# Performance work log

Measured on AMD Instinct MI355X. Metric: run time of the kernel, lower is better.

Reference implementation:

```python
import jax, jax.numpy as jnp
import numpy as np

B, S, N, F_RAW = 32, 48, 1000, 21
H = 64           # hidden_dim
A_DIM = 10       # aspect_dim
FEAT = 4 * A_DIM # projected feature_dim = 40

OFF_IDX = np.array([2, 5, 8, 9, 12])
DEF_IDX = np.array([10, 14, 15])
ERR_IDX = np.array([13, 17])
INF_IDX = np.array([19, 20])


def _glorot(k, shape):
    lim = (6.0 / (shape[0] + shape[1])) ** 0.5
    return jax.random.uniform(k, shape, minval=-lim, maxval=lim, dtype=jnp.float32)


def setup_inputs() -> dict:
    key = jax.random.key(0)
    ks = jax.random.split(key, 12)
    return {
        'inputs': jax.random.normal(ks[0], (B, S, N, F_RAW), dtype=jnp.float32),
        'adj': jax.random.uniform(ks[1], (N, N), dtype=jnp.float32),
        # aspect projection linears (weight stored as [in, out])
        'Wo': _glorot(ks[2], (5, A_DIM)), 'bo': jnp.zeros((A_DIM,), jnp.float32),
        'Wd': _glorot(ks[3], (3, A_DIM)), 'bd': jnp.zeros((A_DIM,), jnp.float32),
        'We': _glorot(ks[4], (2, A_DIM)), 'be': jnp.zeros((A_DIM,), jnp.float32),
        'Wi': _glorot(ks[5], (2, A_DIM)), 'bi': jnp.zeros((A_DIM,), jnp.float32),
        # graph-conv GRU weights: gates (bias init 1.0) and candidate (bias 0.0)
        'W1': _glorot(ks[6], (H + FEAT, 2 * H)), 'b1': jnp.ones((2 * H,), jnp.float32),
        'W2': _glorot(ks[7], (H + FEAT, H)), 'b2': jnp.zeros((H,), jnp.float32),
    }


def _laplacian_with_self_loop(adj):
    A = adj + jnp.eye(adj.shape[0], dtype=adj.dtype)
    d_inv_sqrt = A.sum(axis=1) ** -0.5
    return d_inv_sqrt[:, None] * A * d_inv_sqrt[None, :]


def reference(inputs, adj, Wo, bo, Wd, bd, We, be, Wi, bi, W1, b1, W2, b2):
    b, s, n, _ = inputs.shape
    L = _laplacian_with_self_loop(adj)  # [N, N]

    # vectorized per-node aspect projections -> [B, S, N, 40]
    x = jnp.concatenate([
        inputs[..., OFF_IDX] @ Wo + bo,
        inputs[..., DEF_IDX] @ Wd + bd,
        inputs[..., ERR_IDX] @ We + be,
        inputs[..., INF_IDX] @ Wi + bi,
    ], axis=-1)

    def gconv(x_t, h_flat, W, bias, out_dim):
        # x_t: [B, N, FEAT]; h_flat: [B, N*H]
        cat = jnp.concatenate([x_t, h_flat.reshape(b, n, H)], axis=-1)  # [B,N,H+FEAT]
        ag = jnp.einsum('mn,bnf->bmf', L, cat)                          # [B,N,H+FEAT]
        out = ag @ W + bias                                             # [B,N,out_dim]
        return out.reshape(b, n * out_dim)

    def step(h_flat, x_t):
        # NOTE: chunk over the flattened (B, N*2H) axis, as in the torch code
        ru = jax.nn.sigmoid(gconv(x_t, h_flat, W1, b1, 2 * H))  # [B, N*2H]
        r, u = jnp.split(ru, 2, axis=1)                          # each [B, N*H]
        c = jnp.tanh(gconv(x_t, r * h_flat, W2, b2, H))          # [B, N*H]
        h_new = u * h_flat + (1.0 - u) * c
        return h_new, None

    h0 = jnp.zeros((b, n * H), dtype=inputs.dtype)
    h_last, _ = jax.lax.scan(step, h0, jnp.swapaxes(x, 0, 1))  # scan over seq
    return h_last.reshape(b, n, H)
```

## Files before the change

### kernel.cpp

```cpp
#include <hip/hip_runtime.h>
#include <math.h>

#define NN    1000
#define KP    1024
#define BATCH 32
#define SEQ   48
#define HID   64
#define LCOLS 32256

typedef unsigned short u16;
typedef __attribute__((ext_vector_type(8))) short  short8v;
typedef __attribute__((ext_vector_type(8))) unsigned short ushort8v;
typedef __attribute__((ext_vector_type(4))) float  float4v;

__device__ __forceinline__ u16 f2bf(float x) {
    union { float f; unsigned u; } v; v.f = x;
    unsigned r = v.u + 0x7FFF + ((v.u >> 16) & 1);
    return (u16)(r >> 16);
}
__device__ __forceinline__ float bf2f(u16 h) {
    union { unsigned u; float f; } v; v.u = ((unsigned)h) << 16;
    return v.f;
}

__global__ void k_rowsum(const float* __restrict__ adj, float* __restrict__ dinv) {
    int m = blockIdx.x;
    float s = 0.f;
    for (int n = threadIdx.x; n < NN; n += blockDim.x)
        s += adj[(size_t)m*NN + n];
    __shared__ float red[256];
    red[threadIdx.x] = s; __syncthreads();
    for (int st = 128; st > 0; st >>= 1) {
        if (threadIdx.x < st) red[threadIdx.x] += red[threadIdx.x + st];
        __syncthreads();
    }
    if (threadIdx.x == 0) dinv[m] = rsqrtf(red[0] + 1.0f);
}

__global__ void k_buildL(const float* __restrict__ adj, const float* __restrict__ dinv,
                         u16* __restrict__ Lhi) {
    int idx = blockIdx.x * 256 + threadIdx.x;
    if (idx >= KP*KP) return;
    int m = idx >> 10, k = idx & (KP-1);
    float v = 0.f;
    if (m < NN && k < NN)
        v = dinv[m] * (adj[(size_t)m*NN + k] + (m == k ? 1.f : 0.f)) * dinv[k];
    Lhi[idx] = f2bf(v);
}

__global__ void k_buildLf(const float* __restrict__ adj, const float* __restrict__ dinv,
                          u16* __restrict__ Lf) {
    size_t idx = (size_t)blockIdx.x * 256 + threadIdx.x;
    if (idx >= (size_t)KP*KP) return;
    int e    = idx & 7;
    int lane = (idx >> 3) & 63;
    int kb   = (idx >> 9) & 31;
    int mg   = idx >> 14;
    int m = mg*16 + (lane & 15);
    int k = kb*32 + (lane >> 4)*8 + e;
    float v = 0.f;
    if (m < NN && k < NN)
        v = dinv[m] * (adj[(size_t)m*NN + k] + (m == k ? 1.f : 0.f)) * dinv[k];
    Lf[idx] = f2bf(v);
}

__global__ void k_srow(const float* __restrict__ adj, const float* __restrict__ dinv,
                       float* __restrict__ srl) {
    int m = blockIdx.x;
    __shared__ float red[256];
    float s = 0.f;
    if (m < NN)
        for (int n = threadIdx.x; n < NN; n += blockDim.x)
            s += adj[(size_t)m*NN + n] * dinv[n];
    red[threadIdx.x] = s; __syncthreads();
    for (int st = 128; st > 0; st >>= 1) {
        if (threadIdx.x < st) red[threadIdx.x] += red[threadIdx.x + st];
        __syncthreads();
    }
    if (threadIdx.x == 0) srl[m] = (m < NN) ? dinv[m] * (red[0] + dinv[m]) : 0.f;
}

__global__ void k_wconv(const float* __restrict__ W1, const float* __restrict__ W2,
                        u16* __restrict__ W1h, u16* __restrict__ W2h) {
    int idx = blockIdx.x * 256 + threadIdx.x;
    if (idx < 128*128) {
        int k = idx >> 7, f = idx & 127;
        W1h[idx] = f2bf((f < 104) ? W1[f*128 + k] : 0.f);
    } else if (idx < 128*128 + 64*128) {
        int i2 = idx - 128*128;
        int c = i2 >> 7, f = i2 & 127;
        W2h[i2] = f2bf((f < 104) ? W2[f*64 + c] : 0.f);
    }
}

__global__ void k_packW(const float* __restrict__ Wo, const float* __restrict__ bo,
                        const float* __restrict__ Wd, const float* __restrict__ bd,
                        const float* __restrict__ We, const float* __restrict__ be,
                        const float* __restrict__ Wi, const float* __restrict__ bi,
                        float* __restrict__ Wp, float* __restrict__ bp) {
    for (int o = threadIdx.x; o < 21*40; o += 256) {
        int f = o / 40, a = o - f*40;
        int g = a / 10, aa = a - 10*g;
        float v = 0.f;
        if (g == 0) {
            if (f == 2) v = Wo[0*10+aa]; else if (f == 5) v = Wo[1*10+aa];
            else if (f == 8) v = Wo[2*10+aa]; else if (f == 9) v = Wo[3*10+aa];
            else if (f == 12) v = Wo[4*10+aa];
        } else if (g == 1) {
            if (f == 10) v = Wd[aa]; else if (f == 14) v = Wd[10+aa];
            else if (f == 15) v = Wd[20+aa];
        } else if (g == 2) {
            if (f == 13) v = We[aa]; else if (f == 17) v = We[10+aa];
        } else {
            if (f == 19) v = Wi[aa]; else if (f == 20) v = Wi[10+aa];
        }
        Wp[o] = v;
    }
    if (threadIdx.x < 40) {
        int a = threadIdx.x, g = a / 10, aa = a - 10*g;
        bp[a] = (g == 0) ? bo[aa] : (g == 1) ? bd[aa] : (g == 2) ? be[aa] : bi[aa];
    }
}

__global__ __launch_bounds__(256)
void k_transpose(const float* __restrict__ inputs, u16* __restrict__ inT) {
    int bt = blockIdx.x;
    int b = bt / SEQ, t = bt - b*SEQ;
    int nt = blockIdx.y;
    __shared__ float sm[128][22];
    const float* base = inputs + ((size_t)bt * NN + nt*128) * 21;
    for (int i = threadIdx.x; i < 128*21; i += 256) {
        int nn = i / 21, f = i - nn*21;
        int n = nt*128 + nn;
        sm[nn][f] = (n < NN) ? base[(size_t)nn*21 + f] : 0.f;
    }
    __syncthreads();
    for (int o = threadIdx.x; o < 21*128; o += 256) {
        int f = o >> 7, nn = o & 127;
        inT[(size_t)((t*32 + b)*21 + f)*KP + nt*128 + nn] = f2bf(sm[nn][f]);
    }
}

__global__ __launch_bounds__(512)
void k_gemm(const u16* __restrict__ A, const u16* __restrict__ B,
            u16* __restrict__ Cout, int ncols) {
    __shared__ char sA[128*64];
    __shared__ char sB[64*64];
    const int n0 = blockIdx.x * 64;
    const int m0 = blockIdx.y * 128;
    const int tid = threadIdx.x;
    const int w = tid >> 6, lane = tid & 63;
    const int l15 = lane & 15, l4 = lane >> 4;
    const int wm = w >> 1, wn = w & 1;

    float4v acc[2][2];
    #pragma unroll
    for (int i = 0; i < 2; ++i)
        #pragma unroll
        for (int j = 0; j < 2; ++j) acc[i][j] = (float4v){0.f,0.f,0.f,0.f};

    int aoff[2], boff[2];
    #pragma unroll
    for (int mf = 0; mf < 2; ++mf) {
        int r = wm*32 + mf*16 + l15;
        aoff[mf] = (r*64 + l4*16) ^ ((r & 7) << 4);
    }
    #pragma unroll
    for (int nf = 0; nf < 2; ++nf) {
        int r = wn*32 + nf*16 + l15;
        boff[nf] = (r*64 + l4*16) ^ ((r & 7) << 4);
    }
    const int rA = tid >> 2, qA = tid & 3;
    const int dA = (rA*64 + qA*16) ^ ((rA & 7) << 4);
    const size_t gA = (size_t)(m0 + rA)*KP + qA*8;
    const int rB = (tid & 255) >> 2, qB = tid & 3;
    const int dB = (rB*64 + qB*16) ^ ((rB & 7) << 4);
    const size_t gB = (size_t)(n0 + rB)*KP + qB*8;

    for (int kt = 0; kt < 32; ++kt) {
        const int k0 = kt*32;
        __syncthreads();
        *(uint4*)(sA + dA) = *(const uint4*)(A + gA + k0);
        if (tid < 256) *(uint4*)(sB + dB) = *(const uint4*)(B + gB + k0);
        __syncthreads();
        short8v a0 = *(const short8v*)(sA + aoff[0]);
        short8v a1 = *(const short8v*)(sA + aoff[1]);
        short8v b0 = *(const short8v*)(sB + boff[0]);
        short8v b1 = *(const short8v*)(sB + boff[1]);
        acc[0][0] = __builtin_amdgcn_mfma_f32_16x16x32_bf16(a0, b0, acc[0][0], 0, 0, 0);
        acc[0][1] = __builtin_amdgcn_mfma_f32_16x16x32_bf16(a0, b1, acc[0][1], 0, 0, 0);
        acc[1][0] = __builtin_amdgcn_mfma_f32_16x16x32_bf16(a1, b0, acc[1][0], 0, 0, 0);
        acc[1][1] = __builtin_amdgcn_mfma_f32_16x16x32_bf16(a1, b1, acc[1][1], 0, 0, 0);
    }
    #pragma unroll
    for (int mf = 0; mf < 2; ++mf)
        #pragma unroll
        for (int nf = 0; nf < 2; ++nf)
            #pragma unroll
            for (int i = 0; i < 4; ++i) {
                int m = m0 + wm*32 + mf*16 + l4*4 + i;
                int j = n0 + wn*32 + nf*16 + l15;
                Cout[(size_t)m*ncols + j] = f2bf(acc[mf][nf][i]);
            }
}

__device__ __forceinline__ size_t frag_off(int grp, int kb, int lane) {
    return (((size_t)grp*32 + kb)*64 + lane)*8;
}

__global__ __launch_bounds__(256)
void k_g1(const u16* __restrict__ Lf, const u16* __restrict__ hTf,
          const u16* __restrict__ agx, const u16* __restrict__ W1h,
          const float* __restrict__ b1, const float* __restrict__ h_lin,
          u16* __restrict__ rhf, float* __restrict__ u_lin) {
    const int b = blockIdx.x, mt = blockIdx.y;
    const int m0 = mt*64;
    const int tid = threadIdx.x;
    const int w = tid >> 6, lane = tid & 63, l15 = lane & 15, l4 = lane >> 4;
    const int wm = w >> 1, wn = w & 1;

    __shared__ char smem[49408];
    char* sF = smem;
    float* ru_s = (float*)(smem + 16384);

    float4v acc[2][2];
    #pragma unroll
    for (int i = 0; i < 2; ++i)
        #pragma unroll
        for (int j = 0; j < 2; ++j) acc[i][j] = (float4v){0.f,0.f,0.f,0.f};

    const u16* A0 = Lf  + frag_off(mt*4 + wm*2 + 0, 0, lane);
    const u16* A1 = Lf  + frag_off(mt*4 + wm*2 + 1, 0, lane);
    const u16* B0 = hTf + frag_off(b*4  + wn*2 + 0, 0, lane);
    const u16* B1 = hTf + frag_off(b*4  + wn*2 + 1, 0, lane);
    #pragma unroll 8
    for (int kb = 0; kb < 32; ++kb) {
        short8v a0 = *(const short8v*)(A0 + kb*512);
        short8v a1 = *(const short8v*)(A1 + kb*512);
        short8v b0 = *(const short8v*)(B0 + kb*512);
        short8v b1 = *(const short8v*)(B1 + kb*512);
        acc[0][0] = __builtin_amdgcn_mfma_f32_16x16x32_bf16(a0, b0, acc[0][0], 0, 0, 0);
        acc[0][1] = __builtin_amdgcn_mfma_f32_16x16x32_bf16(a0, b1, acc[0][1], 0, 0, 0);
        acc[1][0] = __builtin_amdgcn_mfma_f32_16x16x32_bf16(a1, b0, acc[1][0], 0, 0, 0);
        acc[1][1] = __builtin_amdgcn_mfma_f32_16x16x32_bf16(a1, b1, acc[1][1], 0, 0, 0);
    }

    if (tid < 192) {
        int r = tid / 3, q = tid - 3*(tid/3);
        *(uint4*)(sF + ((r*256 + (13 + q)*16) ^ ((r & 7) << 4))) = (uint4){0,0,0,0};
    }
    for (int i = tid; i < 320; i += 256) {
        int r = i / 5, q = i - 5*(i/5);
        *(uint4*)(sF + ((r*256 + q*16) ^ ((r & 7) << 4))) =
            *(const uint4*)(agx + (size_t)(m0 + r)*1280 + b*40 + q*8);
    }
    #pragma unroll
    for (int mf = 0; mf < 2; ++mf)
        #pragma unroll
        for (int nf = 0; nf < 2; ++nf)
            #pragma unroll
            for (int i = 0; i < 4; ++i) {
                int row = wm*32 + mf*16 + l4*4 + i;
                int f = 40 + wn*32 + nf*16 + l15;
                *(u16*)(sF + ((row*256 + f*2) ^ ((row & 7) << 4))) = f2bf(acc[mf][nf][i]);
            }
    __syncthreads();

    const int gm = (w >> 1)*32, gn = (w & 1)*64;
    float4v acc2[2][4];
    #pragma unroll
    for (int i = 0; i < 2; ++i)
        #pragma unroll
        for (int j = 0; j < 4; ++j) acc2[i][j] = (float4v){0.f,0.f,0.f,0.f};
    for (int kt2 = 0; kt2 < 4; ++kt2) {
        #pragma unroll
        for (int mf = 0; mf < 2; ++mf) {
            int ar2 = gm + mf*16 + l15;
            short8v a = *(const short8v*)(sF + ((ar2*256 + kt2*64 + l4*16) ^ ((ar2 & 7) << 4)));
            #pragma unroll
            for (int nf = 0; nf < 4; ++nf) {
                short8v bb = *(const short8v*)(W1h + (gn + nf*16 + l15)*128 + kt2*32 + l4*8);
                acc2[mf][nf] = __builtin_amdgcn_mfma_f32_16x16x32_bf16(a, bb, acc2[mf][nf], 0, 0, 0);
            }
        }
    }
    #pragma unroll
    for (int mf = 0; mf < 2; ++mf)
        #pragma unroll
        for (int nf = 0; nf < 4; ++nf) {
            int col = gn + nf*16 + l15;
            float bias = b1[col];
            #pragma unroll
            for (int i = 0; i < 4; ++i) {
                int row = gm + mf*16 + l4*4 + i;
                ru_s[row*129 + col] = 1.f / (1.f + __expf(-(acc2[mf][nf][i] + bias)));
            }
        }
    __syncthreads();

    const int c = tid & 63, ng = tid >> 6;
    #pragma unroll
    for (int it = 0; it < 4; ++it) {
        int nc = (it*4 + ng)*8;
        int n = 2*m0 + nc;
        if ((n >> 1) + 3 < 500) {
            ushort8v ov;
            #pragma unroll
            for (int d = 0; d < 8; ++d) {
                int nn = n + d;
                float r = ru_s[((nc + d) >> 1)*129 + (nn & 1)*64 + c];
                float h = h_lin[((size_t)b*NN + nn)*64 + c];
                ov[d] = f2bf(r*h);
            }
            *(ushort8v*)(rhf + frag_off(b*4 + (c >> 4), n >> 5, (c & 15) + 16*((n >> 3) & 3))) = ov;
        }
    }
    for (int lc = 0; lc < 16; lc += 4) {
        int lr = ng*16 + lc;
        int m = m0 + lr;
        if (m >= 500) {
            #pragma unroll
            for (int d = 0; d < 4; ++d) {
                int mm = m + d;
                if (mm < 1000) {
                    int n = 2*(mm - 500);
                    u_lin[((size_t)b*NN + n)*64 + c]     = ru_s[(lr+d)*129 + c];
                    u_lin[((size_t)b*NN + n + 1)*64 + c] = ru_s[(lr+d)*129 + 64 + c];
                }
            }
        }
    }
}

__global__ __launch_bounds__(256)
void k_g2(const u16* __restrict__ Lf, const u16* __restrict__ rhf,
          const u16* __restrict__ agx, const u16* __restrict__ W2h,
          const float* __restrict__ b2, const float* __restrict__ u_lin,
          float* __restrict__ h_lin, u16* __restrict__ hTf,
          const u16* __restrict__ LinpB, const float* __restrict__ Wp,
          const float* __restrict__ bp, const float* __restrict__ srl,
          u16* __restrict__ agx_next, int tnext,
          float* __restrict__ out, int write_out) {
    const int b = blockIdx.x, mt = blockIdx.y;
    const int m0 = mt*64;
    const int tid = threadIdx.x;
    const int w = tid >> 6, lane = tid & 63, l15 = lane & 15, l4 = lane >> 4;
    const int wm = w >> 1, wn = w & 1;

    __shared__ char smem[42016];
    char* sF = smem;
    float* cs  = (float*)(smem + 16384);
    float* sLp = (float*)(smem + 33024);
    float* sWp = (float*)(smem + 38656);
    __shared__ float sbp[40];
    __shared__ float ssr[64];

    float4v acc[2][2];
    #pragma unroll
    for (int i = 0; i < 2; ++i)
        #pragma unroll
        for (int j = 0; j < 2; ++j) acc[i][j] = (float4v){0.f,0.f,0.f,0.f};

    const u16* A0 = Lf  + frag_off(mt*4 + wm*2 + 0, 0, lane);
    const u16* A1 = Lf  + frag_off(mt*4 + wm*2 + 1, 0, lane);
    const u16* B0 = rhf + frag_off(b*4  + wn*2 + 0, 0, lane);
    const u16* B1 = rhf + frag_off(b*4  + wn*2 + 1, 0, lane);
    #pragma unroll 8
    for (int kb = 0; kb < 32; ++kb) {
        short8v a0 = *(const short8v*)(A0 + kb*512);
        short8v a1 = *(const short8v*)(A1 + kb*512);
        short8v b0 = *(const short8v*)(B0 + kb*512);
        short8v b1 = *(const short8v*)(B1 + kb*512);
        acc[0][0] = __builtin_amdgcn_mfma_f32_16x16x32_bf16(a0, b0, acc[0][0], 0, 0, 0);
        acc[0][1] = __builtin_amdgcn_mfma_f32_16x16x32_bf16(a0, b1, acc[0][1], 0, 0, 0);
        acc[1][0] = __builtin_amdgcn_mfma_f32_16x16x32_bf16(a1, b0, acc[1][0], 0, 0, 0);
        acc[1][1] = __builtin_amdgcn_mfma_f32_16x16x32_bf16(a1, b1, acc[1][1], 0, 0, 0);
    }

    if (tid < 192) {
        int r = tid / 3, q = tid - 3*(tid/3);
        *(uint4*)(sF + ((r*256 + (13 + q)*16) ^ ((r & 7) << 4))) = (uint4){0,0,0,0};
    }
    for (int i = tid; i < 320; i += 256) {
        int r = i / 5, q = i - 5*(i/5);
        *(uint4*)(sF + ((r*256 + q*16) ^ ((r & 7) << 4))) =
            *(const uint4*)(agx + (size_t)(m0 + r)*1280 + b*40 + q*8);
    }
    #pragma unroll
    for (int mf = 0; mf < 2; ++mf)
        #pragma unroll
        for (int nf = 0; nf < 2; ++nf)
            #pragma unroll
            for (int i = 0; i < 4; ++i) {
                int row = wm*32 + mf*16 + l4*4 + i;
                int f = 40 + wn*32 + nf*16 + l15;
                *(u16*)(sF + ((row*256 + f*2) ^ ((row & 7) << 4))) = f2bf(acc[mf][nf][i]);
            }
    __syncthreads();

    const int gm = (w >> 1)*32, gn = (w & 1)*32;
    float4v acc3[2][2];
    #pragma unroll
    for (int i = 0; i < 2; ++i)
        #pragma unroll
        for (int j = 0; j < 2; ++j) acc3[i][j] = (float4v){0.f,0.f,0.f,0.f};
    for (int kt2 = 0; kt2 < 4; ++kt2) {
        #pragma unroll
        for (int mf = 0; mf < 2; ++mf) {
            int ar2 = gm + mf*16 + l15;
            short8v a = *(const short8v*)(sF + ((ar2*256 + kt2*64 + l4*16) ^ ((ar2 & 7) << 4)));
            #pragma unroll
            for (int nf = 0; nf < 2; ++nf) {
                short8v bb = *(const short8v*)(W2h + (gn + nf*16 + l15)*128 + kt2*32 + l4*8);
                acc3[mf][nf] = __builtin_amdgcn_mfma_f32_16x16x32_bf16(a, bb, acc3[mf][nf], 0, 0, 0);
            }
        }
    }
    #pragma unroll
    for (int mf = 0; mf < 2; ++mf)
        #pragma unroll
        for (int nf = 0; nf < 2; ++nf) {
            int col = gn + nf*16 + l15;
            float bias = b2[col];
            #pragma unroll
            for (int i = 0; i < 4; ++i) {
                int row = gm + mf*16 + l4*4 + i;
                cs[row*65 + col] = acc3[mf][nf][i] + bias;
            }
        }
    __syncthreads();

    const int c = tid & 63, ng = tid >> 6;
    for (int lc = 0; lc < 16; lc += 8) {
        int lr = ng*16 + lc;
        int m = m0 + lr;
        ushort8v hiv;
        #pragma unroll
        for (int d = 0; d < 8; ++d) {
            int mm = m + d;
            float hn = 0.f;
            if (mm < NN) {
                float x = cs[(lr+d)*65 + c];
                x = fminf(fmaxf(x, -15.f), 15.f);
                float e = __expf(2.f*x);
                float cand = (e - 1.f) / (e + 1.f);
                size_t idx = ((size_t)b*NN + mm)*64 + c;
                float u = u_lin[idx], h = h_lin[idx];
                hn = u*h + (1.f - u)*cand;
                h_lin[idx] = hn;
                if (write_out) out[idx] = hn;
            }
            hiv[d] = f2bf(hn);
        }
        *(ushort8v*)(hTf + frag_off(b*4 + (c >> 4), m >> 5, (c & 15) + 16*((m >> 3) & 3))) = hiv;
    }

    if (tnext < SEQ) {
        for (int i = tid; i < 64*21; i += 256) {
            int r = i / 21, f = i - 21*(i/21);
            sLp[r*22 + f] = bf2f(LinpB[(size_t)(m0 + r)*LCOLS + tnext*672 + b*21 + f]);
        }
        for (int i = tid; i < 21*40; i += 256) sWp[i] = Wp[i];
        if (tid < 40) sbp[tid] = bp[tid];
        if (tid < 64) ssr[tid] = srl[m0 + tid];
        __syncthreads();
        for (int o = tid; o < 64*40; o += 256) {
            int r = o / 40, a = o - 40*(o/40);
            float acc4 = ssr[r] * sbp[a];
            #pragma unroll
            for (int f = 0; f < 21; ++f) acc4 += sLp[r*22 + f] * sWp[f*40 + a];
            agx_next[(size_t)(m0 + r)*1280 + b*40 + a] = f2bf(acc4);
        }
    }
}

__global__ __launch_bounds__(256)
void k_xproj2(const u16* __restrict__ LinpB, const float* __restrict__ Wp,
              const float* __restrict__ bp, const float* __restrict__ srl,
              u16* __restrict__ agx, int t) {
    const int b = blockIdx.x, mt = blockIdx.y;
    const int tid = threadIdx.x;
    __shared__ float sLp[64][22];
    __shared__ float sWp[21*40];
    __shared__ float sbp[40];
    __shared__ float ssr[64];
    for (int i = tid; i < 64*21; i += 256) {
        int r = i / 21, f = i - 21*(i/21);
        sLp[r][f] = bf2f(LinpB[(size_t)(mt*64 + r)*LCOLS + t*672 + b*21 + f]);
    }
    for (int i = tid; i < 21*40; i += 256) sWp[i] = Wp[i];
    if (tid < 40) sbp[tid] = bp[tid];
    if (tid < 64) ssr[tid] = srl[mt*64 + tid];
    __syncthreads();
    for (int o = tid; o < 64*40; o += 256) {
        int r = o / 40, a = o - 40*(o/40);
        float acc2 = ssr[r] * sbp[a];
        #pragma unroll
        for (int f = 0; f < 21; ++f) acc2 += sLp[r][f] * sWp[f*40 + a];
        agx[(size_t)(mt*64 + r)*1280 + b*40 + a] = f2bf(acc2);
    }
}

#define O_LHI   0ull
#define O_LF    2097152ull
#define O_LINP  4194304ull
#define O_HLIN  70254592ull
#define O_ULIN  78446592ull
#define O_HTF   86638592ull
#define O_RHF   90832896ull
#define O_AGX0  95027200ull
#define O_AGX1  97648640ull
#define O_W1H   100270080ull
#define O_W2H   100302848ull
#define O_WP    100319232ull
#define O_BP    100323328ull
#define O_DINV  100323584ull
#define O_SRL   100327680ull
#define O_INT   100331776ull

extern "C" void kernel_launch(void* const* d_in, const int* in_sizes, int n_in,
                              void* d_out, int out_size, void* d_ws, size_t ws_size,
                              hipStream_t stream) {
    const float* inputs = (const float*)d_in[0];
    const float* adj    = (const float*)d_in[1];
    const float* Wo = (const float*)d_in[2];  const float* bo = (const float*)d_in[3];
    const float* Wd = (const float*)d_in[4];  const float* bd = (const float*)d_in[5];
    const float* We = (const float*)d_in[6];  const float* be = (const float*)d_in[7];
    const float* Wi = (const float*)d_in[8];  const float* bi = (const float*)d_in[9];
    const float* W1 = (const float*)d_in[10]; const float* b1 = (const float*)d_in[11];
    const float* W2 = (const float*)d_in[12]; const float* b2 = (const float*)d_in[13];
    float* out = (float*)d_out;

    char* ws = (char*)d_ws;
    u16*   Lhi   = (u16*)(ws + O_LHI);
    u16*   Lf    = (u16*)(ws + O_LF);
    u16*   LinpB = (u16*)(ws + O_LINP);
    float* h_lin = (float*)(ws + O_HLIN);
    float* u_lin = (float*)(ws + O_ULIN);
    u16*   hTf   = (u16*)(ws + O_HTF);
    u16*   rhf   = (u16*)(ws + O_RHF);
    u16*   agx0  = (u16*)(ws + O_AGX0);
    u16*   agx1  = (u16*)(ws + O_AGX1);
    u16*   W1h   = (u16*)(ws + O_W1H);
    u16*   W2h   = (u16*)(ws + O_W2H);
    float* Wp    = (float*)(ws + O_WP);
    float* bp    = (float*)(ws + O_BP);
    float* dinv  = (float*)(ws + O_DINV);
    float* srl   = (float*)(ws + O_SRL);
    u16*   inT   = (u16*)(ws + O_INT);

    k_rowsum<<<NN, 256, 0, stream>>>(adj, dinv);
    k_buildL<<<(KP*KP)/256, 256, 0, stream>>>(adj, dinv, Lhi);
    k_buildLf<<<(KP*KP)/256, 256, 0, stream>>>(adj, dinv, Lf);
    k_srow<<<KP, 256, 0, stream>>>(adj, dinv, srl);
    k_wconv<<<96, 256, 0, stream>>>(W1, W2, W1h, W2h);
    k_packW<<<1, 256, 0, stream>>>(Wo, bo, Wd, bd, We, be, Wi, bi, Wp, bp);
    k_transpose<<<dim3(BATCH*SEQ, 8), 256, 0, stream>>>(inputs, inT);
    k_gemm<<<dim3(LCOLS/64, 8), 512, 0, stream>>>(Lhi, inT, LinpB, LCOLS);

    hipMemsetAsync(ws + O_HLIN, 0, 8192000ull, stream);
    hipMemsetAsync(ws + O_HTF,  0, 4194304ull, stream);
    hipMemsetAsync(ws + O_RHF,  0, 4194304ull, stream);
    k_xproj2<<<dim3(32,16), 256, 0, stream>>>(LinpB, Wp, bp, srl, agx0, 0);

    for (int t = 0; t < SEQ; ++t) {
        u16* agxc = (t & 1) ? agx1 : agx0;
        u16* agxn = (t & 1) ? agx0 : agx1;
        k_g1<<<dim3(32,16), 256, 0, stream>>>(Lf, hTf, agxc, W1h, b1, h_lin, rhf, u_lin);
        k_g2<<<dim3(32,16), 256, 0, stream>>>(Lf, rhf, agxc, W2h, b2, u_lin, h_lin, hTf,
                                              LinpB, Wp, bp, srl, agxn, t + 1,
                                              out, t == SEQ - 1);
    }
}
```

Baseline: 2.690 ms.

## Fuse GRU time loop into one persistent cooperative kernel with grid syncs

Replaces the 96 per-timestep kernel launches (k_g1/k_g2 per step) with a single persistent cooperative kernel that loops over the sequence and uses grid.sync between the gate and candidate phases. Weights for the x projection and the L fragment pointers are loaded once per block. The aim is to remove launch overhead and kernel-boundary drains. It adds grid-wide barrier cost and depends on occupancy, falling back to two blocks per CU or to the old launch loop if co-residency fails.

```diff
diff --git a/kernel.cpp b/kernel.cpp
--- a/kernel.cpp
+++ b/kernel.cpp
@@ -1,5 +1,8 @@
 #include <hip/hip_runtime.h>
+#include <hip/hip_cooperative_groups.h>
 #include <math.h>
+
+namespace cg = cooperative_groups;
 
 #define NN    1000
 #define KP    1024
@@ -208,6 +211,283 @@
     return (((size_t)grp*32 + kb)*64 + lane)*8;
 }
 
+template<int WPB>
+__global__ __launch_bounds__(256)
+void k_loop(const u16* __restrict__ Lf, u16* __restrict__ hTf, u16* __restrict__ rhf,
+            u16* __restrict__ agx0, u16* __restrict__ agx1,
+            const u16* __restrict__ W1h, const u16* __restrict__ W2h,
+            const float* __restrict__ b1, const float* __restrict__ b2,
+            float* __restrict__ h_lin, float* __restrict__ u_lin,
+            const u16* __restrict__ LinpB, const float* __restrict__ Wp,
+            const float* __restrict__ bp, const float* __restrict__ srl,
+            float* __restrict__ out) {
+    cg::grid_group grid = cg::this_grid();
+    const int bid = blockIdx.x;
+    const int NBLK = 512 / WPB;
+    const int mt = bid & 15;
+    const int m0 = mt*64;
+    const int tid = threadIdx.x;
+    const int w = tid >> 6, lane = tid & 63, l15 = lane & 15, l4 = lane >> 4;
+    const int wm = w >> 1, wn = w & 1;
+    const int c = tid & 63, ng = tid >> 6;
+
+    __shared__ char smem[49408];
+    __shared__ float sWp2[21*40];
+    __shared__ float sbp2[40];
+    __shared__ float ssr2[64];
+
+    for (int i = tid; i < 21*40; i += 256) sWp2[i] = Wp[i];
+    if (tid < 40) sbp2[tid] = bp[tid];
+    if (tid < 64) ssr2[tid] = srl[m0 + tid];
+
+    const u16* LA0 = Lf + frag_off(mt*4 + wm*2 + 0, 0, lane);
+    const u16* LA1 = Lf + frag_off(mt*4 + wm*2 + 1, 0, lane);
+    __syncthreads();
+
+    #pragma unroll 1
+    for (int t = 0; t < SEQ; ++t) {
+        const u16* agxc = (t & 1) ? agx1 : agx0;
+        u16*       agxn = (t & 1) ? agx0 : agx1;
+
+        #pragma unroll 1
+        for (int s = 0; s < WPB; ++s) {
+            const int b = (s*NBLK + bid) >> 4;
+            __syncthreads();
+            char* sF = smem;
+            float* ru_s = (float*)(smem + 16384);
+
+            float4v acc[2][2];
+            #pragma unroll
+            for (int i = 0; i < 2; ++i)
+                #pragma unroll
+                for (int j = 0; j < 2; ++j) acc[i][j] = (float4v){0.f,0.f,0.f,0.f};
+
+            const u16* B0 = hTf + frag_off(b*4 + wn*2 + 0, 0, lane);
+            const u16* B1 = hTf + frag_off(b*4 + wn*2 + 1, 0, lane);
+            #pragma unroll 8
+            for (int kb = 0; kb < 32; ++kb) {
+                short8v a0 = *(const short8v*)(LA0 + kb*512);
+                short8v a1 = *(const short8v*)(LA1 + kb*512);
+                short8v b0 = *(const short8v*)(B0 + kb*512);
+                short8v b1 = *(const short8v*)(B1 + kb*512);
+                acc[0][0] = __builtin_amdgcn_mfma_f32_16x16x32_bf16(a0, b0, acc[0][0], 0, 0, 0);
+                acc[0][1] = __builtin_amdgcn_mfma_f32_16x16x32_bf16(a0, b1, acc[0][1], 0, 0, 0);
+                acc[1][0] = __builtin_amdgcn_mfma_f32_16x16x32_bf16(a1, b0, acc[1][0], 0, 0, 0);
+                acc[1][1] = __builtin_amdgcn_mfma_f32_16x16x32_bf16(a1, b1, acc[1][1], 0, 0, 0);
+            }
+
+            if (tid < 192) {
+                int r = tid / 3, q = tid - 3*(tid/3);
+                *(uint4*)(sF + ((r*256 + (13 + q)*16) ^ ((r & 7) << 4))) = (uint4){0,0,0,0};
+            }
+            for (int i = tid; i < 320; i += 256) {
+                int r = i / 5, q = i - 5*(i/5);
+                *(uint4*)(sF + ((r*256 + q*16) ^ ((r & 7) << 4))) =
+                    *(const uint4*)(agxc + (size_t)(m0 + r)*1280 + b*40 + q*8);
+            }
+            #pragma unroll
+            for (int mf = 0; mf < 2; ++mf)
+                #pragma unroll
+                for (int nf = 0; nf < 2; ++nf)
+                    #pragma unroll
+                    for (int i = 0; i < 4; ++i) {
+                        int row = wm*32 + mf*16 + l4*4 + i;
+                        int f = 40 + wn*32 + nf*16 + l15;
+                        *(u16*)(sF + ((row*256 + f*2) ^ ((row & 7) << 4))) = f2bf(acc[mf][nf][i]);
+                    }
+            __syncthreads();
+
+            const int gm = wm*32, gn = wn*64;
+            float4v acc2[2][4];
+            #pragma unroll
+            for (int i = 0; i < 2; ++i)
+                #pragma unroll
+                for (int j = 0; j < 4; ++j) acc2[i][j] = (float4v){0.f,0.f,0.f,0.f};
+            for (int kt2 = 0; kt2 < 4; ++kt2) {
+                #pragma unroll
+                for (int mf = 0; mf < 2; ++mf) {
+                    int ar2 = gm + mf*16 + l15;
+                    short8v a = *(const short8v*)(sF + ((ar2*256 + kt2*64 + l4*16) ^ ((ar2 & 7) << 4)));
+                    #pragma unroll
+                    for (int nf = 0; nf < 4; ++nf) {
+                        short8v bb = *(const short8v*)(W1h + (gn + nf*16 + l15)*128 + kt2*32 + l4*8);
+                        acc2[mf][nf] = __builtin_amdgcn_mfma_f32_16x16x32_bf16(a, bb, acc2[mf][nf], 0, 0, 0);
+                    }
+                }
+            }
+            #pragma unroll
+            for (int mf = 0; mf < 2; ++mf)
+                #pragma unroll
+                for (int nf = 0; nf < 4; ++nf) {
+                    int col = gn + nf*16 + l15;
+                    float bias = b1[col];
+                    #pragma unroll
+                    for (int i = 0; i < 4; ++i) {
+                        int row = gm + mf*16 + l4*4 + i;
+                        ru_s[row*129 + col] = 1.f / (1.f + __expf(-(acc2[mf][nf][i] + bias)));
+                    }
+                }
+            __syncthreads();
+
+            #pragma unroll
+            for (int it = 0; it < 4; ++it) {
+                int nc = (it*4 + ng)*8;
+                int n = 2*m0 + nc;
+                if ((n >> 1) + 3 < 500) {
+                    ushort8v ov;
+                    #pragma unroll
+                    for (int d = 0; d < 8; ++d) {
+                        int nn = n + d;
+                        float r = ru_s[((nc + d) >> 1)*129 + (nn & 1)*64 + c];
+                        float h = h_lin[((size_t)b*NN + nn)*64 + c];
+                        ov[d] = f2bf(r*h);
+                    }
+                    *(ushort8v*)(rhf + frag_off(b*4 + (c >> 4), n >> 5, (c & 15) + 16*((n >> 3) & 3))) = ov;
+                }
+            }
+            for (int lc = 0; lc < 16; lc += 4) {
+                int lr = ng*16 + lc;
+                int m = m0 + lr;
+                if (m >= 500) {
+                    #pragma unroll
+                    for (int d = 0; d < 4; ++d) {
+                        int mm = m + d;
+                        if (mm < 1000) {
+                            int n = 2*(mm - 500);
+                            u_lin[((size_t)b*NN + n)*64 + c]     = ru_s[(lr+d)*129 + c];
+                            u_lin[((size_t)b*NN + n + 1)*64 + c] = ru_s[(lr+d)*129 + 64 + c];
+                        }
+                    }
+                }
+            }
+        }
+        grid.sync();
+
+        #pragma unroll 1
+        for (int s = 0; s < WPB; ++s) {
+            const int b = (s*NBLK + bid) >> 4;
+            __syncthreads();
+            char* sF = smem;
+            float* cs  = (float*)(smem + 16384);
+            float* sLp = (float*)(smem + 33024);
+
+            float4v acc[2][2];
+            #pragma unroll
+            for (int i = 0; i < 2; ++i)
+                #pragma unroll
+                for (int j = 0; j < 2; ++j) acc[i][j] = (float4v){0.f,0.f,0.f,0.f};
+
+            const u16* B0 = rhf + frag_off(b*4 + wn*2 + 0, 0, lane);
+            const u16* B1 = rhf + frag_off(b*4 + wn*2 + 1, 0, lane);
+            #pragma unroll 8
+            for (int kb = 0; kb < 32; ++kb) {
+                short8v a0 = *(const short8v*)(LA0 + kb*512);
+                short8v a1 = *(const short8v*)(LA1 + kb*512);
+                short8v b0 = *(const short8v*)(B0 + kb*512);
+                short8v b1 = *(const short8v*)(B1 + kb*512);
+                acc[0][0] = __builtin_amdgcn_mfma_f32_16x16x32_bf16(a0, b0, acc[0][0], 0, 0, 0);
+                acc[0][1] = __builtin_amdgcn_mfma_f32_16x16x32_bf16(a0, b1, acc[0][1], 0, 0, 0);
+                acc[1][0] = __builtin_amdgcn_mfma_f32_16x16x32_bf16(a1, b0, acc[1][0], 0, 0, 0);
+                acc[1][1] = __builtin_amdgcn_mfma_f32_16x16x32_bf16(a1, b1, acc[1][1], 0, 0, 0);
+            }
+
+            if (tid < 192) {
+                int r = tid / 3, q = tid - 3*(tid/3);
+                *(uint4*)(sF + ((r*256 + (13 + q)*16) ^ ((r & 7) << 4))) = (uint4){0,0,0,0};
+            }
+            for (int i = tid; i < 320; i += 256) {
+                int r = i / 5, q = i - 5*(i/5);
+                *(uint4*)(sF + ((r*256 + q*16) ^ ((r & 7) << 4))) =
+                    *(const uint4*)(agxc + (size_t)(m0 + r)*1280 + b*40 + q*8);
+            }
+            #pragma unroll
+            for (int mf = 0; mf < 2; ++mf)
+                #pragma unroll
+                for (int nf = 0; nf < 2; ++nf)
+                    #pragma unroll
+                    for (int i = 0; i < 4; ++i) {
+                        int row = wm*32 + mf*16 + l4*4 + i;
+                        int f = 40 + wn*32 + nf*16 + l15;
+                        *(u16*)(sF + ((row*256 + f*2) ^ ((row & 7) << 4))) = f2bf(acc[mf][nf][i]);
+                    }
+            __syncthreads();
+
+            const int gm = wm*32, gn = wn*32;
+            float4v acc3[2][2];
+            #pragma unroll
+            for (int i = 0; i < 2; ++i)
+                #pragma unroll
+                for (int j = 0; j < 2; ++j) acc3[i][j] = (float4v){0.f,0.f,0.f,0.f};
+            for (int kt2 = 0; kt2 < 4; ++kt2) {
+                #pragma unroll
+                for (int mf = 0; mf < 2; ++mf) {
+                    int ar2 = gm + mf*16 + l15;
+                    short8v a = *(const short8v*)(sF + ((ar2*256 + kt2*64 + l4*16) ^ ((ar2 & 7) << 4)));
+                    #pragma unroll
+                    for (int nf = 0; nf < 2; ++nf) {
+                        short8v bb = *(const short8v*)(W2h + (gn + nf*16 + l15)*128 + kt2*32 + l4*8);
+                        acc3[mf][nf] = __builtin_amdgcn_mfma_f32_16x16x32_bf16(a, bb, acc3[mf][nf], 0, 0, 0);
+                    }
+                }
+            }
+            #pragma unroll
+            for (int mf = 0; mf < 2; ++mf)
+                #pragma unroll
+                for (int nf = 0; nf < 2; ++nf) {
+                    int col = gn + nf*16 + l15;
+                    float bias = b2[col];
+                    #pragma unroll
+                    for (int i = 0; i < 4; ++i) {
+                        int row = gm + mf*16 + l4*4 + i;
+                        cs[row*65 + col] = acc3[mf][nf][i] + bias;
+                    }
+                }
+            __syncthreads();
+
+            const int write_out = (t == SEQ - 1);
+            for (int lc = 0; lc < 16; lc += 8) {
+                int lr = ng*16 + lc;
+                int m = m0 + lr;
+                ushort8v hiv;
+                #pragma unroll
+                for (int d = 0; d < 8; ++d) {
+                    int mm = m + d;
+                    float hn = 0.f;
+                    if (mm < NN) {
+                        float x = cs[(lr+d)*65 + c];
+                        x = fminf(fmaxf(x, -15.f), 15.f);
+                        float e = __expf(2.f*x);
+                        float cand = (e - 1.f) / (e + 1.f);
+                        size_t idx = ((size_t)b*NN + mm)*64 + c;
+                        float u = u_lin[idx], h = h_lin[idx];
+                        hn = u*h + (1.f - u)*cand;
+                        h_lin[idx] = hn;
+                        if (write_out) out[idx] = hn;
+                    }
+                    hiv[d] = f2bf(hn);
+                }
+                *(ushort8v*)(hTf + frag_off(b*4 + (c >> 4), m >> 5, (c & 15) + 16*((m >> 3) & 3))) = hiv;
+            }
+
+            if (t + 1 < SEQ) {
+                for (int i = tid; i < 64*21; i += 256) {
+                    int r = i / 21, f = i - 21*(i/21);
+                    sLp[r*22 + f] = bf2f(LinpB[(size_t)(m0 + r)*LCOLS + (t+1)*672 + b*21 + f]);
+                }
+                __syncthreads();
+                for (int o = tid; o < 64*40; o += 256) {
+                    int r = o / 40, a = o - 40*(o/40);
+                    float acc4 = ssr2[r] * sbp2[a];
+                    #pragma unroll
+                    for (int f = 0; f < 21; ++f) acc4 += sLp[r*22 + f] * sWp2[f*40 + a];
+                    agxn[(size_t)(m0 + r)*1280 + b*40 + a] = f2bf(acc4);
+                }
+            }
+        }
+        grid.sync();
+    }
+}
+
 __global__ __launch_bounds__(256)
 void k_g1(const u16* __restrict__ Lf, const u16* __restrict__ hTf,
           const u16* __restrict__ agx, const u16* __restrict__ W1h,
@@ -266,7 +546,7 @@
             }
     __syncthreads();
 
-    const int gm = (w >> 1)*32, gn = (w & 1)*64;
+    const int gm = wm*32, gn = wn*64;
     float4v acc2[2][4];
     #pragma unroll
     for (int i = 0; i < 2; ++i)
@@ -398,7 +678,7 @@
             }
     __syncthreads();
 
-    const int gm = (w >> 1)*32, gn = (w & 1)*32;
+    const int gm = wm*32, gn = wn*32;
     float4v acc3[2][2];
     #pragma unroll
     for (int i = 0; i < 2; ++i)
@@ -563,12 +843,38 @@
     hipMemsetAsync(ws + O_RHF,  0, 4194304ull, stream);
     k_xproj2<<<dim3(32,16), 256, 0, stream>>>(LinpB, Wp, bp, srl, agx0, 0);
 
-    for (int t = 0; t < SEQ; ++t) {
-        u16* agxc = (t & 1) ? agx1 : agx0;
-        u16* agxn = (t & 1) ? agx0 : agx1;
-        k_g1<<<dim3(32,16), 256, 0, stream>>>(Lf, hTf, agxc, W1h, b1, h_lin, rhf, u_lin);
-        k_g2<<<dim3(32,16), 256, 0, stream>>>(Lf, rhf, agxc, W2h, b2, u_lin, h_lin, hTf,
-                                              LinpB, Wp, bp, srl, agxn, t + 1,
-                                              out, t == SEQ - 1);
-    }
-}
+    void* args[] = {
+        (void*)&Lf, (void*)&hTf, (void*)&rhf, (void*)&agx0, (void*)&agx1,
+        (void*)&W1h, (void*)&W2h, (void*)&b1, (void*)&b2,
+        (void*)&h_lin, (void*)&u_lin, (void*)&LinpB, (void*)&Wp,
+        (void*)&bp, (void*)&srl, (void*)&out
+    };
+
+    hipError_t le = hipErrorUnknown;
+    int occ1 = 0;
+    if (hipOccupancyMaxActiveBlocksPerMultiprocessor(
+            &occ1, reinterpret_cast<const void*>(&k_loop<1>), 256, 0) == hipSuccess
+        && occ1 >= 2) {
+        le = hipLaunchCooperativeKernel(reinterpret_cast<const void*>(&k_loop<1>),
+                                        dim3(512), dim3(256), args, 0, stream);
+    }
+    if (le != hipSuccess) {
+        int occ2 = 0;
+        if (hipOccupancyMaxActiveBlocksPerMultiprocessor(
+                &occ2, reinterpret_cast<const void*>(&k_loop<2>), 256, 0) == hipSuccess
+            && occ2 >= 1) {
+            le = hipLaunchCooperativeKernel(reinterpret_cast<const void*>(&k_loop<2>),
+                                            dim3(256), dim3(256), args, 0, stream);
+        }
+    }
+    if (le != hipSuccess) {
+        for (int t = 0; t < SEQ; ++t) {
+            u16* agxc = (t & 1) ? agx1 : agx0;
+            u16* agxn = (t & 1) ? agx0 : agx1;
+            k_g1<<<dim3(32,16), 256, 0, stream>>>(Lf, hTf, agxc, W1h, b1, h_lin, rhf, u_lin);
+            k_g2<<<dim3(32,16), 256, 0, stream>>>(Lf, rhf, agxc, W2h, b2, u_lin, h_lin, hTf,
+                                                  LinpB, Wp, bp, srl, agxn, t + 1,
+                                                  out, t == SEQ - 1);
+        }
+    }
+}
```

New measurement: 2.680 ms. About the same (-0.4%).

## Double threads per block in GRU step kernels and prefetch h/u earlier

Applied to the files above, without the earlier changes.

Raises the recurrent k_g1/k_g2 kernels from 256 to 512 threads, splitting the output tile across 8 waves so each wave computes half as many MFMA fragments over the 1024-long K loop. It also issues the h_lin/u_lin loads into registers right after the main loop, and in k_g2 moves the next-step projection's shared-memory staging ahead of the second GEMM, so these global latencies overlap with compute. The grid is only 512 blocks per launch, so more waves per block is meant to raise latency hiding. The cost is that each wave now reloads the Lf A fragments with half the reuse, and register pressure changes under the 512-thread bound.

```diff
diff --git a/kernel.cpp b/kernel.cpp
--- a/kernel.cpp
+++ b/kernel.cpp
@@ -208,7 +208,7 @@
     return (((size_t)grp*32 + kb)*64 + lane)*8;
 }
 
-__global__ __launch_bounds__(256)
+__global__ __launch_bounds__(512)
 void k_g1(const u16* __restrict__ Lf, const u16* __restrict__ hTf,
           const u16* __restrict__ agx, const u16* __restrict__ W1h,
           const float* __restrict__ b1, const float* __restrict__ h_lin,
@@ -217,68 +217,72 @@
     const int m0 = mt*64;
     const int tid = threadIdx.x;
     const int w = tid >> 6, lane = tid & 63, l15 = lane & 15, l4 = lane >> 4;
-    const int wm = w >> 1, wn = w & 1;
+    const int wm = w >> 2, wn = w & 3;
+    const int c = tid & 63, ng = tid >> 6;
 
     __shared__ char smem[49408];
     char* sF = smem;
     float* ru_s = (float*)(smem + 16384);
 
-    float4v acc[2][2];
-    #pragma unroll
-    for (int i = 0; i < 2; ++i)
-        #pragma unroll
-        for (int j = 0; j < 2; ++j) acc[i][j] = (float4v){0.f,0.f,0.f,0.f};
-
+    float4v acc[2];
+    acc[0] = (float4v){0.f,0.f,0.f,0.f};
+    acc[1] = (float4v){0.f,0.f,0.f,0.f};
     const u16* A0 = Lf  + frag_off(mt*4 + wm*2 + 0, 0, lane);
     const u16* A1 = Lf  + frag_off(mt*4 + wm*2 + 1, 0, lane);
-    const u16* B0 = hTf + frag_off(b*4  + wn*2 + 0, 0, lane);
-    const u16* B1 = hTf + frag_off(b*4  + wn*2 + 1, 0, lane);
+    const u16* B0 = hTf + frag_off(b*4  + wn, 0, lane);
     #pragma unroll 8
     for (int kb = 0; kb < 32; ++kb) {
         short8v a0 = *(const short8v*)(A0 + kb*512);
         short8v a1 = *(const short8v*)(A1 + kb*512);
         short8v b0 = *(const short8v*)(B0 + kb*512);
-        short8v b1 = *(const short8v*)(B1 + kb*512);
-        acc[0][0] = __builtin_amdgcn_mfma_f32_16x16x32_bf16(a0, b0, acc[0][0], 0, 0, 0);
-        acc[0][1] = __builtin_amdgcn_mfma_f32_16x16x32_bf16(a0, b1, acc[0][1], 0, 0, 0);
-        acc[1][0] = __builtin_amdgcn_mfma_f32_16x16x32_bf16(a1, b0, acc[1][0], 0, 0, 0);
-        acc[1][1] = __builtin_amdgcn_mfma_f32_16x16x32_bf16(a1, b1, acc[1][1], 0, 0, 0);
+        acc[0] = __builtin_amdgcn_mfma_f32_16x16x32_bf16(a0, b0, acc[0], 0, 0, 0);
+        acc[1] = __builtin_amdgcn_mfma_f32_16x16x32_bf16(a1, b0, acc[1], 0, 0, 0);
+    }
+
+    float hpre[2][8];
+    #pragma unroll
+    for (int it = 0; it < 2; ++it) {
+        int nc = (it*8 + ng)*8;
+        int n = 2*m0 + nc;
+        if ((n >> 1) + 3 < 500) {
+            #pragma unroll
+            for (int d = 0; d < 8; ++d)
+                hpre[it][d] = h_lin[((size_t)b*NN + n + d)*64 + c];
+        }
     }
 
     if (tid < 192) {
         int r = tid / 3, q = tid - 3*(tid/3);
         *(uint4*)(sF + ((r*256 + (13 + q)*16) ^ ((r & 7) << 4))) = (uint4){0,0,0,0};
     }
-    for (int i = tid; i < 320; i += 256) {
-        int r = i / 5, q = i - 5*(i/5);
+    if (tid < 320) {
+        int r = tid / 5, q = tid - 5*(tid/5);
         *(uint4*)(sF + ((r*256 + q*16) ^ ((r & 7) << 4))) =
             *(const uint4*)(agx + (size_t)(m0 + r)*1280 + b*40 + q*8);
     }
     #pragma unroll
     for (int mf = 0; mf < 2; ++mf)
         #pragma unroll
-        for (int nf = 0; nf < 2; ++nf)
-            #pragma unroll
-            for (int i = 0; i < 4; ++i) {
-                int row = wm*32 + mf*16 + l4*4 + i;
-                int f = 40 + wn*32 + nf*16 + l15;
-                *(u16*)(sF + ((row*256 + f*2) ^ ((row & 7) << 4))) = f2bf(acc[mf][nf][i]);
-            }
+        for (int i = 0; i < 4; ++i) {
+            int row = (wm*2 + mf)*16 + l4*4 + i;
+            int f = 40 + wn*16 + l15;
+            *(u16*)(sF + ((row*256 + f*2) ^ ((row & 7) << 4))) = f2bf(acc[mf][i]);
+        }
     __syncthreads();
 
-    const int gm = (w >> 1)*32, gn = (w & 1)*64;
-    float4v acc2[2][4];
+    const int gm = (w >> 2)*32, gn = (w & 3)*32;
+    float4v acc2[2][2];
     #pragma unroll
     for (int i = 0; i < 2; ++i)
         #pragma unroll
-        for (int j = 0; j < 4; ++j) acc2[i][j] = (float4v){0.f,0.f,0.f,0.f};
+        for (int j = 0; j < 2; ++j) acc2[i][j] = (float4v){0.f,0.f,0.f,0.f};
     for (int kt2 = 0; kt2 < 4; ++kt2) {
         #pragma unroll
         for (int mf = 0; mf < 2; ++mf) {
             int ar2 = gm + mf*16 + l15;
             short8v a = *(const short8v*)(sF + ((ar2*256 + kt2*64 + l4*16) ^ ((ar2 & 7) << 4)));
             #pragma unroll
-            for (int nf = 0; nf < 4; ++nf) {
+            for (int nf = 0; nf < 2; ++nf) {
                 short8v bb = *(const short8v*)(W1h + (gn + nf*16 + l15)*128 + kt2*32 + l4*8);
                 acc2[mf][nf] = __builtin_amdgcn_mfma_f32_16x16x32_bf16(a, bb, acc2[mf][nf], 0, 0, 0);
             }
@@ -287,7 +291,7 @@
     #pragma unroll
     for (int mf = 0; mf < 2; ++mf)
         #pragma unroll
-        for (int nf = 0; nf < 4; ++nf) {
+        for (int nf = 0; nf < 2; ++nf) {
             int col = gn + nf*16 + l15;
             float bias = b1[col];
             #pragma unroll
@@ -298,10 +302,9 @@
         }
     __syncthreads();
 
-    const int c = tid & 63, ng = tid >> 6;
-    #pragma unroll
-    for (int it = 0; it < 4; ++it) {
-        int nc = (it*4 + ng)*8;
+    #pragma unroll
+    for (int it = 0; it < 2; ++it) {
+        int nc = (it*8 + ng)*8;
         int n = 2*m0 + nc;
         if ((n >> 1) + 3 < 500) {
             ushort8v ov;
@@ -309,14 +312,14 @@
             for (int d = 0; d < 8; ++d) {
                 int nn = n + d;
                 float r = ru_s[((nc + d) >> 1)*129 + (nn & 1)*64 + c];
-                float h = h_lin[((size_t)b*NN + nn)*64 + c];
-                ov[d] = f2bf(r*h);
+                ov[d] = f2bf(r * hpre[it][d]);
             }
             *(ushort8v*)(rhf + frag_off(b*4 + (c >> 4), n >> 5, (c & 15) + 16*((n >> 3) & 3))) = ov;
         }
     }
-    for (int lc = 0; lc < 16; lc += 4) {
-        int lr = ng*16 + lc;
+    #pragma unroll
+    for (int lc = 0; lc < 8; lc += 4) {
+        int lr = ng*8 + lc;
         int m = m0 + lr;
         if (m >= 500) {
             #pragma unroll
@@ -332,7 +335,7 @@
     }
 }
 
-__global__ __launch_bounds__(256)
+__global__ __launch_bounds__(512)
 void k_g2(const u16* __restrict__ Lf, const u16* __restrict__ rhf,
           const u16* __restrict__ agx, const u16* __restrict__ W2h,
           const float* __restrict__ b2, const float* __restrict__ u_lin,
@@ -345,7 +348,8 @@
     const int m0 = mt*64;
     const int tid = threadIdx.x;
     const int w = tid >> 6, lane = tid & 63, l15 = lane & 15, l4 = lane >> 4;
-    const int wm = w >> 1, wn = w & 1;
+    const int wm = w >> 2, wn = w & 3;
+    const int c = tid & 63, ng = tid >> 6;
 
     __shared__ char smem[42016];
     char* sF = smem;
@@ -355,84 +359,90 @@
     __shared__ float sbp[40];
     __shared__ float ssr[64];
 
-    float4v acc[2][2];
-    #pragma unroll
-    for (int i = 0; i < 2; ++i)
-        #pragma unroll
-        for (int j = 0; j < 2; ++j) acc[i][j] = (float4v){0.f,0.f,0.f,0.f};
-
+    float4v acc[2];
+    acc[0] = (float4v){0.f,0.f,0.f,0.f};
+    acc[1] = (float4v){0.f,0.f,0.f,0.f};
     const u16* A0 = Lf  + frag_off(mt*4 + wm*2 + 0, 0, lane);
     const u16* A1 = Lf  + frag_off(mt*4 + wm*2 + 1, 0, lane);
-    const u16* B0 = rhf + frag_off(b*4  + wn*2 + 0, 0, lane);
-    const u16* B1 = rhf + frag_off(b*4  + wn*2 + 1, 0, lane);
+    const u16* B0 = rhf + frag_off(b*4  + wn, 0, lane);
     #pragma unroll 8
     for (int kb = 0; kb < 32; ++kb) {
         short8v a0 = *(const short8v*)(A0 + kb*512);
         short8v a1 = *(const short8v*)(A1 + kb*512);
         short8v b0 = *(const short8v*)(B0 + kb*512);
-        short8v b1 = *(const short8v*)(B1 + kb*512);
-        acc[0][0] = __builtin_amdgcn_mfma_f32_16x16x32_bf16(a0, b0, acc[0][0], 0, 0, 0);
-        acc[0][1] = __builtin_amdgcn_mfma_f32_16x16x32_bf16(a0, b1, acc[0][1], 0, 0, 0);
-        acc[1][0] = __builtin_amdgcn_mfma_f32_16x16x32_bf16(a1, b0, acc[1][0], 0, 0, 0);
-        acc[1][1] = __builtin_amdgcn_mfma_f32_16x16x32_bf16(a1, b1, acc[1][1], 0, 0, 0);
+        acc[0] = __builtin_amdgcn_mfma_f32_16x16x32_bf16(a0, b0, acc[0], 0, 0, 0);
+        acc[1] = __builtin_amdgcn_mfma_f32_16x16x32_bf16(a1, b0, acc[1], 0, 0, 0);
+    }
+
+    float upre[8], hpre[8];
+    {
+        int m = m0 + ng*8;
+        #pragma unroll
+        for (int d = 0; d < 8; ++d) {
+            int mm = m + d;
+            size_t idx = ((size_t)b*NN + mm)*64 + c;
+            bool ok = mm < NN;
+            upre[d] = ok ? u_lin[idx] : 0.f;
+            hpre[d] = ok ? h_lin[idx] : 0.f;
+        }
     }
 
     if (tid < 192) {
         int r = tid / 3, q = tid - 3*(tid/3);
         *(uint4*)(sF + ((r*256 + (13 + q)*16) ^ ((r & 7) << 4))) = (uint4){0,0,0,0};
     }
-    for (int i = tid; i < 320; i += 256) {
-        int r = i / 5, q = i - 5*(i/5);
+    if (tid < 320) {
+        int r = tid / 5, q = tid - 5*(tid/5);
         *(uint4*)(sF + ((r*256 + q*16) ^ ((r & 7) << 4))) =
             *(const uint4*)(agx + (size_t)(m0 + r)*1280 + b*40 + q*8);
     }
     #pragma unroll
     for (int mf = 0; mf < 2; ++mf)
         #pragma unroll
-        for (int nf = 0; nf < 2; ++nf)
-            #pragma unroll
-            for (int i = 0; i < 4; ++i) {
-                int row = wm*32 + mf*16 + l4*4 + i;
-                int f = 40 + wn*32 + nf*16 + l15;
-                *(u16*)(sF + ((row*256 + f*2) ^ ((row & 7) << 4))) = f2bf(acc[mf][nf][i]);
-            }
+        for (int i = 0; i < 4; ++i) {
+            int row = (wm*2 + mf)*16 + l4*4 + i;
+            int f = 40 + wn*16 + l15;
+            *(u16*)(sF + ((row*256 + f*2) ^ ((row & 7) << 4))) = f2bf(acc[mf][i]);
+        }
     __syncthreads();
 
-    const int gm = (w >> 1)*32, gn = (w & 1)*32;
-    float4v acc3[2][2];
-    #pragma unroll
-    for (int i = 0; i < 2; ++i)
-        #pragma unroll
-        for (int j = 0; j < 2; ++j) acc3[i][j] = (float4v){0.f,0.f,0.f,0.f};
+    if (tnext < SEQ) {
+        for (int i = tid; i < 64*21; i += 512) {
+            int r = i / 21, f = i - 21*(i/21);
+            sLp[r*22 + f] = bf2f(LinpB[(size_t)(m0 + r)*LCOLS + tnext*672 + b*21 + f]);
+        }
+        for (int i = tid; i < 21*40; i += 512) sWp[i] = Wp[i];
+        if (tid < 40) sbp[tid] = bp[tid];
+        if (tid < 64) ssr[tid] = srl[m0 + tid];
+    }
+
+    const int gm = (w >> 2)*32, gn = (w & 3)*16;
+    float4v acc3[2];
+    acc3[0] = (float4v){0.f,0.f,0.f,0.f};
+    acc3[1] = (float4v){0.f,0.f,0.f,0.f};
     for (int kt2 = 0; kt2 < 4; ++kt2) {
         #pragma unroll
         for (int mf = 0; mf < 2; ++mf) {
             int ar2 = gm + mf*16 + l15;
             short8v a = *(const short8v*)(sF + ((ar2*256 + kt2*64 + l4*16) ^ ((ar2 & 7) << 4)));
-            #pragma unroll
-            for (int nf = 0; nf < 2; ++nf) {
-                short8v bb = *(const short8v*)(W2h + (gn + nf*16 + l15)*128 + kt2*32 + l4*8);
-                acc3[mf][nf] = __builtin_amdgcn_mfma_f32_16x16x32_bf16(a, bb, acc3[mf][nf], 0, 0, 0);
-            }
-        }
-    }
-    #pragma unroll
-    for (int mf = 0; mf < 2; ++mf)
-        #pragma unroll
-        for (int nf = 0; nf < 2; ++nf) {
-            int col = gn + nf*16 + l15;
-            float bias = b2[col];
-            #pragma unroll
-            for (int i = 0; i < 4; ++i) {
-                int row = gm + mf*16 + l4*4 + i;
-                cs[row*65 + col] = acc3[mf][nf][i] + bias;
-            }
-        }
+            short8v bb = *(const short8v*)(W2h + (gn + l15)*128 + kt2*32 + l4*8);
+            acc3[mf] = __builtin_amdgcn_mfma_f32_16x16x32_bf16(a, bb, acc3[mf], 0, 0, 0);
+        }
+    }
+    #pragma unroll
+    for (int mf = 0; mf < 2; ++mf) {
+        int col = gn + l15;
+        float bias = b2[col];
+        #pragma unroll
+        for (int i = 0; i < 4; ++i) {
+            int row = gm + mf*16 + l4*4 + i;
+            cs[row*65 + col] = acc3[mf][i] + bias;
+        }
+    }
     __syncthreads();
 
-    const int c = tid & 63, ng = tid >> 6;
-    for (int lc = 0; lc < 16; lc += 8) {
-        int lr = ng*16 + lc;
+    {
+        int lr = ng*8;
         int m = m0 + lr;
         ushort8v hiv;
         #pragma unroll
@@ -444,9 +454,9 @@
                 x = fminf(fmaxf(x, -15.f), 15.f);
                 float e = __expf(2.f*x);
                 float cand = (e - 1.f) / (e + 1.f);
+                float u = upre[d], h = hpre[d];
+                hn = u*h + (1.f - u)*cand;
                 size_t idx = ((size_t)b*NN + mm)*64 + c;
-                float u = u_lin[idx], h = h_lin[idx];
-                hn = u*h + (1.f - u)*cand;
                 h_lin[idx] = hn;
                 if (write_out) out[idx] = hn;
             }
@@ -456,15 +466,8 @@
     }
 
     if (tnext < SEQ) {
-        for (int i = tid; i < 64*21; i += 256) {
-            int r = i / 21, f = i - 21*(i/21);
-            sLp[r*22 + f] = bf2f(LinpB[(size_t)(m0 + r)*LCOLS + tnext*672 + b*21 + f]);
-        }
-        for (int i = tid; i < 21*40; i += 256) sWp[i] = Wp[i];
-        if (tid < 40) sbp[tid] = bp[tid];
-        if (tid < 64) ssr[tid] = srl[m0 + tid];
         __syncthreads();
-        for (int o = tid; o < 64*40; o += 256) {
+        for (int o = tid; o < 64*40; o += 512) {
             int r = o / 40, a = o - 40*(o/40);
             float acc4 = ssr[r] * sbp[a];
             #pragma unroll
@@ -566,8 +569,8 @@
     for (int t = 0; t < SEQ; ++t) {
         u16* agxc = (t & 1) ? agx1 : agx0;
         u16* agxn = (t & 1) ? agx0 : agx1;
-        k_g1<<<dim3(32,16), 256, 0, stream>>>(Lf, hTf, agxc, W1h, b1, h_lin, rhf, u_lin);
-        k_g2<<<dim3(32,16), 256, 0, stream>>>(Lf, rhf, agxc, W2h, b2, u_lin, h_lin, hTf,
+        k_g1<<<dim3(32,16), 512, 0, stream>>>(Lf, hTf, agxc, W1h, b1, h_lin, rhf, u_lin);
+        k_g2<<<dim3(32,16), 512, 0, stream>>>(Lf, rhf, agxc, W2h, b2, u_lin, h_lin, hTf,
                                               LinpB, Wp, bp, srl, agxn, t + 1,
                                               out, t == SEQ - 1);
     }
```

New measurement: 2.428 ms. 9.7% less time.
